# Performance work log

Hardware: AMD Instinct MI355X
Metric: run time of the kernel (lower is better)

Reference implementation:

```python
import jax, jax.numpy as jnp
import numpy as np

NEG_SLOPE = 0.2  # LeakyReLU slope used by GAT attention
EPS = 1e-16


def gat_conv(x, edge_index, W, a_src, a_dst, b):
    """One GATConv layer with 'mean' head aggregation.
    x: [N, Fin], edge_index: [2, E] (row 0 = src/j, row 1 = dst/i),
    W: [Fin, H*F], a_src/a_dst: [H, F], b: [F].
    Returns [N, F].
    """
    N = x.shape[0]
    H, F = a_src.shape
    h = (x @ W).reshape(N, H, F)                      # [N, H, F]
    src, dst = edge_index[0], edge_index[1]
    # per-node attention halves, gathered per edge
    as_ = jnp.einsum('nhf,hf->nh', h, a_src)          # [N, H]
    ad_ = jnp.einsum('nhf,hf->nh', h, a_dst)          # [N, H]
    e = jax.nn.leaky_relu(as_[src] + ad_[dst], NEG_SLOPE)  # [E, H]
    # segment softmax over incoming edges of each dst node
    m = jax.ops.segment_max(e, dst, num_segments=N)   # [N, H]
    ex = jnp.exp(e - m[dst])                          # [E, H]
    denom = jax.ops.segment_sum(ex, dst, num_segments=N)
    alpha = ex / (denom[dst] + EPS)                   # [E, H]
    # weighted scatter-aggregate of source features
    out = jax.ops.segment_sum(alpha[:, :, None] * h[src], dst, num_segments=N)  # [N, H, F]
    return out.mean(axis=1) + b                       # mean over heads


def setup_inputs() -> dict:
    key = jax.random.key(0)
    ks = jax.random.split(key, 10)
    N, E = 100000, 1000000
    in_dim, hid, out_dim, H = 128, 32, 16, 4
    x = jax.random.normal(ks[0], (N, in_dim), dtype=jnp.float32)
    edge_index = jax.random.randint(ks[1], (2, E), 0, N, dtype=jnp.int64)
    s1 = 1.0 / np.sqrt(in_dim)
    s2 = 1.0 / np.sqrt(hid)
    W1 = jax.random.uniform(ks[2], (in_dim, H * hid), jnp.float32, -s1, s1)
    a1_src = jax.random.uniform(ks[3], (H, hid), jnp.float32, -s2, s2)
    a1_dst = jax.random.uniform(ks[4], (H, hid), jnp.float32, -s2, s2)
    b1 = jnp.zeros((hid,), jnp.float32)
    s3 = 1.0 / np.sqrt(out_dim)
    W2 = jax.random.uniform(ks[5], (hid, H * out_dim), jnp.float32, -s2, s2)
    a2_src = jax.random.uniform(ks[6], (H, out_dim), jnp.float32, -s3, s3)
    a2_dst = jax.random.uniform(ks[7], (H, out_dim), jnp.float32, -s3, s3)
    b2 = jnp.zeros((out_dim,), jnp.float32)
    return {"x": x, "edge_index": edge_index,
            "W1": W1, "a1_src": a1_src, "a1_dst": a1_dst, "b1": b1,
            "W2": W2, "a2_src": a2_src, "a2_dst": a2_dst, "b2": b2}


def reference(x, edge_index, W1, a1_src, a1_dst, b1, W2, a2_src, a2_dst, b2):
    h = gat_conv(x, edge_index, W1, a1_src, a1_dst, b1)
    h = jax.nn.relu(h)
    # dropout is identity in eval mode
    out = gat_conv(h, edge_index, W2, a2_src, a2_dst, b2)
    return out
```

## Files before the change

kernel.cpp:

```cpp
#include <hip/hip_runtime.h>
#include <math.h>

#define NEG_SLOPE 0.2f
#define EPS_GAT 1e-16f
#define LOG2E 1.4426950408889634f
typedef unsigned int u32;
typedef unsigned short u16;
typedef __attribute__((ext_vector_type(8))) short short8;
typedef __attribute__((ext_vector_type(4))) float f32x4;

__device__ inline u16 f2bf(float x) {
    union { float f; u32 u; } v; v.f = x;
    u32 r = v.u + 0x7FFFu + ((v.u >> 16) & 1u);
    return (u16)(r >> 16);
}
__device__ inline float bf_lo(u32 u) {
    union { u32 i; float f; } v; v.i = u << 16; return v.f;
}
__device__ inline float bf_hi(u32 u) {
    union { u32 i; float f; } v; v.i = u & 0xFFFF0000u; return v.f;
}
__device__ inline float bf1(u16 s) {
    union { u32 i; float f; } v; v.i = ((u32)s) << 16; return v.f;
}
__device__ inline float fast_exp2(float x) {
#if __has_builtin(__builtin_amdgcn_exp2f)
    return __builtin_amdgcn_exp2f(x);
#else
    return exp2f(x);
#endif
}
__device__ inline float lrelu_exp2(float t) {
    return fast_exp2(fmaxf(t, NEG_SLOPE * t));
}


__global__ void degree_prep_kernel(const int* __restrict__ dst, int E,
                                   int* __restrict__ counts, int* __restrict__ rank,
                                   const float* __restrict__ W1,
                                   u16* __restrict__ w1t_hi, u16* __restrict__ w1t_lo,
                                   const float* __restrict__ W2, const float* __restrict__ a2s,
                                   const float* __restrict__ a2d, float* __restrict__ w_as,
                                   float* __restrict__ w_ad, int degBlocks) {
    int b = blockIdx.x;
    if (b < degBlocks) {
        int e = b * 256 + threadIdx.x;
        if (e < E) rank[e] = atomicAdd(&counts[dst[e]], 1);
    } else if (b < degBlocks + 64) {
        int i = (b - degBlocks) * 256 + threadIdx.x;
        int k = i >> 7, n = i & 127;
        float w = W1[i];
        u16 hi = f2bf(w);
        u16 lo = f2bf(w - bf1(hi));
        w1t_hi[n * 128 + k] = hi;
        w1t_lo[n * 128 + k] = lo;
    } else {
        int t = threadIdx.x;
        if (t < 128) {
            int h = t >> 5, k = t & 31;
            float s1 = 0.f, s2 = 0.f;
#pragma unroll
            for (int f = 0; f < 16; ++f) {
                float w = W2[k * 64 + h * 16 + f];
                s1 += w * a2s[h * 16 + f];
                s2 += w * a2d[h * 16 + f];
            }
            w_as[h * 32 + k] = s1;
            w_ad[h * 32 + k] = s2;
        }
    }
}

__global__ __launch_bounds__(1024) void scan_block_kernel(const int* __restrict__ counts, int N,
                                                          int* __restrict__ scanned, int* __restrict__ bsums) {
    __shared__ int tmp[1024];
    int i = blockIdx.x * 1024 + threadIdx.x;
    int v = (i < N) ? counts[i] : 0;
    tmp[threadIdx.x] = v;
    __syncthreads();
    for (int d = 1; d < 1024; d <<= 1) {
        int t = (threadIdx.x >= d) ? tmp[threadIdx.x - d] : 0;
        __syncthreads();
        tmp[threadIdx.x] += t;
        __syncthreads();
    }
    if (i < N) scanned[i] = tmp[threadIdx.x];
    if (threadIdx.x == 1023) bsums[blockIdx.x] = tmp[1023];
}

__global__ __launch_bounds__(256) void scan_partials_kernel(int* __restrict__ bsums, int nb) {
    __shared__ int tmp[256];
    int tid = threadIdx.x;
    int v = (tid < nb) ? bsums[tid] : 0;
    tmp[tid] = v;
    __syncthreads();
    for (int d = 1; d < 256; d <<= 1) {
        int t = (tid >= d) ? tmp[tid - d] : 0;
        __syncthreads();
        tmp[tid] += t;
        __syncthreads();
    }
    if (tid < nb) bsums[tid] = tmp[tid] - v;
}

__global__ void finalize_offsets_kernel(const int* __restrict__ scanned,
                                        const int* __restrict__ bsums_excl, int N,
                                        int* __restrict__ row_off) {
    int i = blockIdx.x * blockDim.x + threadIdx.x;
    if (i < N) {
        int incl = scanned[i] + bsums_excl[i >> 10];
        row_off[i + 1] = incl;
        if (i == 0) row_off[0] = 0;
    }
}

__global__ void fill_csr_kernel(const int* __restrict__ src, const int* __restrict__ dst, int E,
                                const int* __restrict__ row_off, const int* __restrict__ rank,
                                int* __restrict__ csr_src) {
    int e = blockIdx.x * blockDim.x + threadIdx.x;
    if (e < E) {
        int pos = row_off[dst[e]] + rank[e];
        csr_src[pos] = src[e];
    }
}


__global__ __launch_bounds__(256) void gemm1_mfma_kernel(const float* __restrict__ X,
                                                         const u16* __restrict__ w1t_hi,
                                                         const u16* __restrict__ w1t_lo,
                                                         const float* __restrict__ a_src,
                                                         const float* __restrict__ a_dst,
                                                         u16* __restrict__ Hb,
                                                         float* __restrict__ as_,
                                                         float* __restrict__ ad_, int N) {
    __shared__ u16 xsh_hi[64][40];
    __shared__ u16 xsh_lo[64][40];
    __shared__ u16 wbuf[10240];
    __shared__ float ash[128], adsh[128];
    u16* wsh_hi = wbuf;
    u16* wsh_lo = wbuf + 5120;
    int tid = threadIdx.x;
    int wave = tid >> 6, lane = tid & 63, quad = lane >> 4;
    int m0 = blockIdx.x * 64;

    if (tid < 128) { ash[tid] = a_src[tid]; adsh[tid] = a_dst[tid]; }

    f32x4 acc[4][2];
#pragma unroll
    for (int rt = 0; rt < 4; ++rt)
#pragma unroll
        for (int ct = 0; ct < 2; ++ct) acc[rt][ct] = (f32x4)(0.f);

    int xrow = tid >> 2, xkq = (tid & 3) * 8;

    for (int k0 = 0; k0 < 128; k0 += 32) {
        {
            int gr = m0 + xrow;
            float f[8];
            *(float4*)&f[0] = (gr < N) ? *(const float4*)(X + (size_t)gr * 128 + k0 + xkq)
                                       : make_float4(0.f, 0.f, 0.f, 0.f);
            *(float4*)&f[4] = (gr < N) ? *(const float4*)(X + (size_t)gr * 128 + k0 + xkq + 4)
                                       : make_float4(0.f, 0.f, 0.f, 0.f);
            u16 hi[8], lo[8];
#pragma unroll
            for (int i = 0; i < 8; ++i) {
                hi[i] = f2bf(f[i]);
                lo[i] = f2bf(f[i] - bf1(hi[i]));
            }
            *(uint4*)&xsh_hi[xrow][xkq] = *(uint4*)hi;
            *(uint4*)&xsh_lo[xrow][xkq] = *(uint4*)lo;
        }
        {
#pragma unroll
            for (int i = 0; i < 2; ++i) {
                int id = tid * 2 + i;
                int n = id >> 2, part = id & 3;
                *(uint4*)&wsh_hi[n * 40 + part * 8] =
                    ((const uint4*)(w1t_hi + n * 128 + k0))[part];
                *(uint4*)&wsh_lo[n * 40 + part * 8] =
                    ((const uint4*)(w1t_lo + n * 128 + k0))[part];
            }
        }
        __syncthreads();

        short8 bhi[2], blo[2];
#pragma unroll
        for (int ct = 0; ct < 2; ++ct) {
            int n = wave * 32 + ct * 16 + (lane & 15);
            bhi[ct] = *(const short8*)&wsh_hi[n * 40 + quad * 8];
            blo[ct] = *(const short8*)&wsh_lo[n * 40 + quad * 8];
        }
#pragma unroll
        for (int rt = 0; rt < 4; ++rt) {
            int m = rt * 16 + (lane & 15);
            short8 ahi = *(const short8*)&xsh_hi[m][quad * 8];
            short8 alo = *(const short8*)&xsh_lo[m][quad * 8];
#pragma unroll
            for (int ct = 0; ct < 2; ++ct) {
                acc[rt][ct] = __builtin_amdgcn_mfma_f32_16x16x32_bf16(ahi, bhi[ct], acc[rt][ct], 0, 0, 0);
                acc[rt][ct] = __builtin_amdgcn_mfma_f32_16x16x32_bf16(alo, bhi[ct], acc[rt][ct], 0, 0, 0);
                acc[rt][ct] = __builtin_amdgcn_mfma_f32_16x16x32_bf16(ahi, blo[ct], acc[rt][ct], 0, 0, 0);
            }
        }
        __syncthreads();
    }

    const int HS = 130;
#pragma unroll
    for (int rt = 0; rt < 4; ++rt)
#pragma unroll
        for (int ct = 0; ct < 2; ++ct) {
            int col = wave * 32 + ct * 16 + (lane & 15);
#pragma unroll
            for (int r = 0; r < 4; ++r) {
                int row = rt * 16 + quad * 4 + r;
                u16 hv = f2bf(acc[rt][ct][r]);
                int gr = m0 + row;
                if (gr < N) Hb[(size_t)gr * 128 + col] = hv;
                wbuf[row * HS + col] = hv;
            }
        }
    __syncthreads();

    {
        int row = tid >> 2, h = tid & 3;
        int gr = m0 + row;
        if (gr < N) {
            const u32* hr = (const u32*)&wbuf[row * HS + h * 32];
            float s1 = 0.f, s2 = 0.f;
#pragma unroll
            for (int q = 0; q < 16; ++q) {
                u32 u = hr[q];
                float flo = bf_lo(u), fhi = bf_hi(u);
                s1 += flo * ash[h * 32 + 2 * q] + fhi * ash[h * 32 + 2 * q + 1];
                s2 += flo * adsh[h * 32 + 2 * q] + fhi * adsh[h * 32 + 2 * q + 1];
            }
            as_[(size_t)gr * 4 + h] = s1 * LOG2E;
            ad_[(size_t)gr * 4 + h] = s2 * LOG2E;
        }
    }
}


__global__ __launch_bounds__(256) void node_agg128_kernel(const u32* __restrict__ Hb,
                                                          const float* __restrict__ as_,
                                                          const float* __restrict__ ad_,
                                                          const int* __restrict__ row_off,
                                                          const int* __restrict__ csr_src,
                                                          const float* __restrict__ bias,
                                                          const float* __restrict__ w_as,
                                                          const float* __restrict__ w_ad,
                                                          u32* __restrict__ O1,
                                                          float* __restrict__ as2,
                                                          float* __restrict__ ad2, int N) {
    int lane = threadIdx.x & 63;
    int node = __builtin_amdgcn_readfirstlane(blockIdx.x * 4 + (threadIdx.x >> 6));
    if (node >= N) return;
    int start = __builtin_amdgcn_readfirstlane(row_off[node]);
    int end   = __builtin_amdgcn_readfirstlane(row_off[node + 1]);
    int deg = end - start;
    int h = lane >> 4;
    int r = lane & 15;
    int grpbase = lane & 48;
    float adh = ad_[node * 4 + h];

    int clamp = (deg > 0) ? deg - 1 : 0;
    int vidx = (deg > 0) ? csr_src[start + min(lane, clamp)] : 0;
    int m = min(deg, 64);

    float Pv[4];
#pragma unroll
    for (int q = 0; q < 4; ++q) {
        int eq = q * 16 + r;
        int sq = __shfl(vidx, eq);
        float aq = as_[sq * 4 + h];
        float pe = lrelu_exp2(aq + adh);
        Pv[q] = (eq < m) ? pe : 0.f;
    }
    float den = (Pv[0] + Pv[1]) + (Pv[2] + Pv[3]);
    den += __shfl_xor(den, 1);
    den += __shfl_xor(den, 2);
    den += __shfl_xor(den, 4);
    den += __shfl_xor(den, 8);

    float2 acc = make_float2(0.f, 0.f);
    int j = 0;
#pragma unroll
    for (int q = 0; q < 4; ++q) {
        const int lim = min(m, (q + 1) * 16);
        for (; j + 4 <= lim; j += 4) {
            int s0 = __builtin_amdgcn_readlane(vidx, j);
            int s1 = __builtin_amdgcn_readlane(vidx, j + 1);
            int s2 = __builtin_amdgcn_readlane(vidx, j + 2);
            int s3 = __builtin_amdgcn_readlane(vidx, j + 3);
            float e0 = __shfl(Pv[q], grpbase | (j - q * 16));
            float e1 = __shfl(Pv[q], grpbase | (j + 1 - q * 16));
            float e2 = __shfl(Pv[q], grpbase | (j + 2 - q * 16));
            float e3 = __shfl(Pv[q], grpbase | (j + 3 - q * 16));
            u32 u0 = Hb[(size_t)s0 * 64 + lane];
            u32 u1 = Hb[(size_t)s1 * 64 + lane];
            u32 u2 = Hb[(size_t)s2 * 64 + lane];
            u32 u3 = Hb[(size_t)s3 * 64 + lane];
            acc.x = fmaf(e0, bf_lo(u0), acc.x); acc.y = fmaf(e0, bf_hi(u0), acc.y);
            acc.x = fmaf(e1, bf_lo(u1), acc.x); acc.y = fmaf(e1, bf_hi(u1), acc.y);
            acc.x = fmaf(e2, bf_lo(u2), acc.x); acc.y = fmaf(e2, bf_hi(u2), acc.y);
            acc.x = fmaf(e3, bf_lo(u3), acc.x); acc.y = fmaf(e3, bf_hi(u3), acc.y);
        }
        for (; j < lim; ++j) {
            int s = __builtin_amdgcn_readlane(vidx, j);
            float e = __shfl(Pv[q], grpbase | (j - q * 16));
            u32 u = Hb[(size_t)s * 64 + lane];
            acc.x = fmaf(e, bf_lo(u), acc.x); acc.y = fmaf(e, bf_hi(u), acc.y);
        }
    }
    for (int jj = start + 64; jj < end; ++jj) {
        int s = __builtin_amdgcn_readfirstlane(csr_src[jj]);
        float e = lrelu_exp2(as_[s * 4 + h] + adh);
        u32 u = Hb[(size_t)s * 64 + lane];
        acc.x = fmaf(e, bf_lo(u), acc.x); acc.y = fmaf(e, bf_hi(u), acc.y); den += e;
    }
    float inv = 1.f / (den + EPS_GAT);
    float px = acc.x * inv, py = acc.y * inv;
    px += __shfl_xor(px, 16); py += __shfl_xor(py, 16);
    px += __shfl_xor(px, 32); py += __shfl_xor(py, 32);

    int f2 = (lane & 15) * 2;
    float2 bv = *(const float2*)&bias[f2];
    float ox = fmaxf(px * 0.25f + bv.x, 0.f);
    float oy = fmaxf(py * 0.25f + bv.y, 0.f);
    if (lane < 16)
        O1[node * 16 + lane] = (u32)f2bf(ox) | ((u32)f2bf(oy) << 16);

    int h2 = lane >> 4;
    float2 wa = *(const float2*)&w_as[h2 * 32 + f2];
    float2 wd = *(const float2*)&w_ad[h2 * 32 + f2];
    float ta = ox * wa.x + oy * wa.y;
    float td = ox * wd.x + oy * wd.y;
    ta += __shfl_xor(ta, 1); td += __shfl_xor(td, 1);
    ta += __shfl_xor(ta, 2); td += __shfl_xor(td, 2);
    ta += __shfl_xor(ta, 4); td += __shfl_xor(td, 4);
    ta += __shfl_xor(ta, 8); td += __shfl_xor(td, 8);
    if ((lane & 15) == 0) {
        as2[node * 4 + h2] = ta * LOG2E;
        ad2[node * 4 + h2] = td * LOG2E;
    }
}


__global__ __launch_bounds__(256) void node_agg32_fused_kernel(const u32* __restrict__ O1,
                                                               const float* __restrict__ as_,
                                                               const float* __restrict__ ad_,
                                                               const int* __restrict__ row_off,
                                                               const int* __restrict__ csr_src,
                                                               const float* __restrict__ W2,
                                                               const float* __restrict__ b2,
                                                               float* __restrict__ Out, int N) {
    int lane = threadIdx.x & 63;
    int h = lane >> 4, f = lane & 15;
    int grpbase = lane & 48;
    int node = __builtin_amdgcn_readfirstlane(blockIdx.x * 4 + (threadIdx.x >> 6));
    if (node >= N) return;

    float wcol[32];
#pragma unroll
    for (int k = 0; k < 32; ++k) wcol[k] = W2[k * 64 + lane];
    float bo = b2[f];

    int start = __builtin_amdgcn_readfirstlane(row_off[node]);
    int end   = __builtin_amdgcn_readfirstlane(row_off[node + 1]);
    int deg = end - start;
    float adh = ad_[node * 4 + h];

    int clamp = (deg > 0) ? deg - 1 : 0;
    int vidx = (deg > 0) ? csr_src[start + min(lane, clamp)] : 0;
    int m = min(deg, 64);

    float Pv[4];
#pragma unroll
    for (int q = 0; q < 4; ++q) {
        int eq = q * 16 + f;
        int sq = __shfl(vidx, eq);
        float aq = as_[sq * 4 + h];
        float pe = lrelu_exp2(aq + adh);
        Pv[q] = (eq < m) ? pe : 0.f;
    }
    float den = (Pv[0] + Pv[1]) + (Pv[2] + Pv[3]);
    den += __shfl_xor(den, 1);
    den += __shfl_xor(den, 2);
    den += __shfl_xor(den, 4);
    den += __shfl_xor(den, 8);

    float2 acc = make_float2(0.f, 0.f);
    int j = 0;
#pragma unroll
    for (int q = 0; q < 4; ++q) {
        const int lim = min(m, (q + 1) * 16);
        for (; j + 4 <= lim; j += 4) {
            int s0 = __builtin_amdgcn_readlane(vidx, j);
            int s1 = __builtin_amdgcn_readlane(vidx, j + 1);
            int s2 = __builtin_amdgcn_readlane(vidx, j + 2);
            int s3 = __builtin_amdgcn_readlane(vidx, j + 3);
            float e0 = __shfl(Pv[q], grpbase | (j - q * 16));
            float e1 = __shfl(Pv[q], grpbase | (j + 1 - q * 16));
            float e2 = __shfl(Pv[q], grpbase | (j + 2 - q * 16));
            float e3 = __shfl(Pv[q], grpbase | (j + 3 - q * 16));
            u32 u0 = O1[s0 * 16 + f];
            u32 u1 = O1[s1 * 16 + f];
            u32 u2 = O1[s2 * 16 + f];
            u32 u3 = O1[s3 * 16 + f];
            acc.x = fmaf(e0, bf_lo(u0), acc.x); acc.y = fmaf(e0, bf_hi(u0), acc.y);
            acc.x = fmaf(e1, bf_lo(u1), acc.x); acc.y = fmaf(e1, bf_hi(u1), acc.y);
            acc.x = fmaf(e2, bf_lo(u2), acc.x); acc.y = fmaf(e2, bf_hi(u2), acc.y);
            acc.x = fmaf(e3, bf_lo(u3), acc.x); acc.y = fmaf(e3, bf_hi(u3), acc.y);
        }
        for (; j < lim; ++j) {
            int s = __builtin_amdgcn_readlane(vidx, j);
            float e = __shfl(Pv[q], grpbase | (j - q * 16));
            u32 u = O1[s * 16 + f];
            acc.x = fmaf(e, bf_lo(u), acc.x); acc.y = fmaf(e, bf_hi(u), acc.y);
        }
    }
    for (int jj = start + 64; jj < end; ++jj) {
        int s = __builtin_amdgcn_readfirstlane(csr_src[jj]);
        float e = lrelu_exp2(as_[s * 4 + h] + adh);
        u32 u = O1[s * 16 + f];
        acc.x = fmaf(e, bf_lo(u), acc.x); acc.y = fmaf(e, bf_hi(u), acc.y);
        den += e;
    }
    float inv = 1.f / (den + EPS_GAT);
    float px = acc.x * inv, py = acc.y * inv;

    float s = 0.f;
#pragma unroll
    for (int k = 0; k < 16; ++k) {
        float vx = __shfl(px, grpbase | k);
        float vy = __shfl(py, grpbase | k);
        s = fmaf(vx, wcol[2 * k], s);
        s = fmaf(vy, wcol[2 * k + 1], s);
    }
    s += __shfl_xor(s, 16);
    s += __shfl_xor(s, 32);
    if (lane < 16)
        Out[(size_t)node * 16 + f] = s * 0.25f + bo;
}


extern "C" void kernel_launch(void* const* d_in, const int* in_sizes, int n_in,
                              void* d_out, int out_size, void* d_ws, size_t ws_size,
                              hipStream_t stream) {
    const float* x      = (const float*)d_in[0];
    const int*   eidx   = (const int*)d_in[1];
    const float* W1     = (const float*)d_in[2];
    const float* a1_src = (const float*)d_in[3];
    const float* a1_dst = (const float*)d_in[4];
    const float* b1     = (const float*)d_in[5];
    const float* W2     = (const float*)d_in[6];
    const float* a2_src = (const float*)d_in[7];
    const float* a2_dst = (const float*)d_in[8];
    const float* b2     = (const float*)d_in[9];
    float* out = (float*)d_out;

    const int N = in_sizes[0] / 128;
    const int E = in_sizes[1] / 2;
    const int* src = eidx;
    const int* dst = eidx + E;

    char* base = (char*)d_ws;
    size_t off = 0;
    auto carve = [&](size_t bytes) -> char* {
        off = (off + 255) & ~(size_t)255;
        char* p = base + off;
        off += bytes;
        return p;
    };
    int* counts   = (int*)carve((size_t)N * 4);
    int* scanned  = (int*)carve((size_t)N * 4);
    int* bsums    = (int*)carve(256 * 4);
    int* row_off  = (int*)carve((size_t)(N + 1) * 4);
    int* rank     = (int*)carve((size_t)E * 4);
    int* csr_src  = (int*)carve((size_t)E * 4);
    u16* w1t_hi   = (u16*)carve(128 * 128 * 2);
    u16* w1t_lo   = (u16*)carve(128 * 128 * 2);
    u16* h1b      = (u16*)carve((size_t)N * 128 * 2);
    u32* out1b    = (u32*)carve((size_t)N * 16 * 4);
    float* as1  = (float*)carve((size_t)N * 4 * 4);
    float* ad1  = (float*)carve((size_t)N * 4 * 4);
    float* as2  = (float*)carve((size_t)N * 4 * 4);
    float* ad2  = (float*)carve((size_t)N * 4 * 4);
    float* w_as = (float*)carve(4 * 32 * 4);
    float* w_ad = (float*)carve(4 * 32 * 4);
    (void)ws_size; (void)n_in; (void)out_size;

    hipMemsetAsync(counts, 0, (size_t)N * 4, stream);
    int degBlocks = (E + 255) / 256;
    degree_prep_kernel<<<degBlocks + 65, 256, 0, stream>>>(dst, E, counts, rank,
                                                           W1, w1t_hi, w1t_lo,
                                                           W2, a2_src, a2_dst, w_as, w_ad,
                                                           degBlocks);
    int nb = (N + 1023) / 1024;
    scan_block_kernel<<<nb, 1024, 0, stream>>>(counts, N, scanned, bsums);
    scan_partials_kernel<<<1, 256, 0, stream>>>(bsums, nb);
    finalize_offsets_kernel<<<(N + 255) / 256, 256, 0, stream>>>(scanned, bsums, N, row_off);
    fill_csr_kernel<<<(E + 255) / 256, 256, 0, stream>>>(src, dst, E, row_off, rank, csr_src);

    gemm1_mfma_kernel<<<(N + 63) / 64, 256, 0, stream>>>(x, w1t_hi, w1t_lo, a1_src, a1_dst,
                                                         h1b, as1, ad1, N);
    node_agg128_kernel<<<(N + 3) / 4, 256, 0, stream>>>((const u32*)h1b, as1, ad1,
                                                        row_off, csr_src, b1, w_as, w_ad,
                                                        out1b, as2, ad2, N);

    node_agg32_fused_kernel<<<(N + 3) / 4, 256, 0, stream>>>(out1b, as2, ad2, row_off,
                                                             csr_src, W2, b2, out, N);
}
```

Measured before the change: 315.5 us.

## Specialize low-degree aggregation paths and stage W2 in shared memory

Both aggregation kernels get fast paths for nodes with up to 8 or up to 16 in-edges. These paths compute only the first quarter of attention scores and issue eight gathers back-to-back before accumulating, which puts more loads in flight and skips the unused score slots. Nodes with higher degree keep the original general loop. In the second-layer kernel, the 32-register per-lane copy of W2 is replaced by a block-wide copy of W2 in LDS, read during the output projection. This is meant to cut register pressure and raise occupancy, at the cost of a barrier and extra LDS traffic per block.

```diff
diff --git a/kernel.cpp b/kernel.cpp
--- a/kernel.cpp
+++ b/kernel.cpp
@@ -268,57 +268,96 @@
     int vidx = (deg > 0) ? csr_src[start + min(lane, clamp)] : 0;
     int m = min(deg, 64);
 
-    float Pv[4];
-#pragma unroll
-    for (int q = 0; q < 4; ++q) {
-        int eq = q * 16 + r;
-        int sq = __shfl(vidx, eq);
+    float Pv0;
+    {
+        int sq = __shfl(vidx, r);
         float aq = as_[sq * 4 + h];
         float pe = lrelu_exp2(aq + adh);
-        Pv[q] = (eq < m) ? pe : 0.f;
-    }
-    float den = (Pv[0] + Pv[1]) + (Pv[2] + Pv[3]);
+        Pv0 = (r < m) ? pe : 0.f;
+    }
+    float den = Pv0;
     den += __shfl_xor(den, 1);
     den += __shfl_xor(den, 2);
     den += __shfl_xor(den, 4);
     den += __shfl_xor(den, 8);
 
     float2 acc = make_float2(0.f, 0.f);
-    int j = 0;
-#pragma unroll
-    for (int q = 0; q < 4; ++q) {
-        const int lim = min(m, (q + 1) * 16);
-        for (; j + 4 <= lim; j += 4) {
-            int s0 = __builtin_amdgcn_readlane(vidx, j);
-            int s1 = __builtin_amdgcn_readlane(vidx, j + 1);
-            int s2 = __builtin_amdgcn_readlane(vidx, j + 2);
-            int s3 = __builtin_amdgcn_readlane(vidx, j + 3);
-            float e0 = __shfl(Pv[q], grpbase | (j - q * 16));
-            float e1 = __shfl(Pv[q], grpbase | (j + 1 - q * 16));
-            float e2 = __shfl(Pv[q], grpbase | (j + 2 - q * 16));
-            float e3 = __shfl(Pv[q], grpbase | (j + 3 - q * 16));
-            u32 u0 = Hb[(size_t)s0 * 64 + lane];
-            u32 u1 = Hb[(size_t)s1 * 64 + lane];
-            u32 u2 = Hb[(size_t)s2 * 64 + lane];
-            u32 u3 = Hb[(size_t)s3 * 64 + lane];
-            acc.x = fmaf(e0, bf_lo(u0), acc.x); acc.y = fmaf(e0, bf_hi(u0), acc.y);
-            acc.x = fmaf(e1, bf_lo(u1), acc.x); acc.y = fmaf(e1, bf_hi(u1), acc.y);
-            acc.x = fmaf(e2, bf_lo(u2), acc.x); acc.y = fmaf(e2, bf_hi(u2), acc.y);
-            acc.x = fmaf(e3, bf_lo(u3), acc.x); acc.y = fmaf(e3, bf_hi(u3), acc.y);
-        }
-        for (; j < lim; ++j) {
-            int s = __builtin_amdgcn_readlane(vidx, j);
-            float e = __shfl(Pv[q], grpbase | (j - q * 16));
+
+#define AGG128_BLK8(J0)                                                           \
+    {                                                                             \
+        int sj[8]; u32 uj[8];                                                     \
+        _Pragma("unroll") for (int j = 0; j < 8; ++j)                             \
+            sj[j] = __builtin_amdgcn_readlane(vidx, (J0) + j);                    \
+        _Pragma("unroll") for (int j = 0; j < 8; ++j)                             \
+            uj[j] = Hb[(size_t)sj[j] * 64 + lane];                                \
+        _Pragma("unroll") for (int j = 0; j < 8; ++j) {                           \
+            float e = __shfl(Pv0, grpbase | ((J0) + j));                          \
+            acc.x = fmaf(e, bf_lo(uj[j]), acc.x);                                 \
+            acc.y = fmaf(e, bf_hi(uj[j]), acc.y);                                 \
+        }                                                                         \
+    }
+
+    if (m <= 8) {
+        AGG128_BLK8(0)
+    } else if (m <= 16) {
+        AGG128_BLK8(0)
+        AGG128_BLK8(8)
+    } else {
+        float Pv[4];
+        Pv[0] = Pv0;
+#pragma unroll
+        for (int q = 1; q < 4; ++q) {
+            int eq = q * 16 + r;
+            int sq = __shfl(vidx, eq);
+            float aq = as_[sq * 4 + h];
+            float pe = lrelu_exp2(aq + adh);
+            Pv[q] = (eq < m) ? pe : 0.f;
+        }
+        float d2 = Pv[1] + Pv[2] + Pv[3];
+        d2 += __shfl_xor(d2, 1);
+        d2 += __shfl_xor(d2, 2);
+        d2 += __shfl_xor(d2, 4);
+        d2 += __shfl_xor(d2, 8);
+        den += d2;
+
+        int j = 0;
+#pragma unroll
+        for (int q = 0; q < 4; ++q) {
+            const int lim = min(m, (q + 1) * 16);
+            for (; j + 4 <= lim; j += 4) {
+                int s0 = __builtin_amdgcn_readlane(vidx, j);
+                int s1 = __builtin_amdgcn_readlane(vidx, j + 1);
+                int s2 = __builtin_amdgcn_readlane(vidx, j + 2);
+                int s3 = __builtin_amdgcn_readlane(vidx, j + 3);
+                float e0 = __shfl(Pv[q], grpbase | (j - q * 16));
+                float e1 = __shfl(Pv[q], grpbase | (j + 1 - q * 16));
+                float e2 = __shfl(Pv[q], grpbase | (j + 2 - q * 16));
+                float e3 = __shfl(Pv[q], grpbase | (j + 3 - q * 16));
+                u32 u0 = Hb[(size_t)s0 * 64 + lane];
+                u32 u1 = Hb[(size_t)s1 * 64 + lane];
+                u32 u2 = Hb[(size_t)s2 * 64 + lane];
+                u32 u3 = Hb[(size_t)s3 * 64 + lane];
+                acc.x = fmaf(e0, bf_lo(u0), acc.x); acc.y = fmaf(e0, bf_hi(u0), acc.y);
+                acc.x = fmaf(e1, bf_lo(u1), acc.x); acc.y = fmaf(e1, bf_hi(u1), acc.y);
+                acc.x = fmaf(e2, bf_lo(u2), acc.x); acc.y = fmaf(e2, bf_hi(u2), acc.y);
+                acc.x = fmaf(e3, bf_lo(u3), acc.x); acc.y = fmaf(e3, bf_hi(u3), acc.y);
+            }
+            for (; j < lim; ++j) {
+                int s = __builtin_amdgcn_readlane(vidx, j);
+                float e = __shfl(Pv[q], grpbase | (j - q * 16));
+                u32 u = Hb[(size_t)s * 64 + lane];
+                acc.x = fmaf(e, bf_lo(u), acc.x); acc.y = fmaf(e, bf_hi(u), acc.y);
+            }
+        }
+        for (int jj = start + 64; jj < end; ++jj) {
+            int s = __builtin_amdgcn_readfirstlane(csr_src[jj]);
+            float e = lrelu_exp2(as_[s * 4 + h] + adh);
             u32 u = Hb[(size_t)s * 64 + lane];
-            acc.x = fmaf(e, bf_lo(u), acc.x); acc.y = fmaf(e, bf_hi(u), acc.y);
-        }
-    }
-    for (int jj = start + 64; jj < end; ++jj) {
-        int s = __builtin_amdgcn_readfirstlane(csr_src[jj]);
-        float e = lrelu_exp2(as_[s * 4 + h] + adh);
-        u32 u = Hb[(size_t)s * 64 + lane];
-        acc.x = fmaf(e, bf_lo(u), acc.x); acc.y = fmaf(e, bf_hi(u), acc.y); den += e;
-    }
+            acc.x = fmaf(e, bf_lo(u), acc.x); acc.y = fmaf(e, bf_hi(u), acc.y); den += e;
+        }
+    }
+#undef AGG128_BLK8
+
     float inv = 1.f / (den + EPS_GAT);
     float px = acc.x * inv, py = acc.y * inv;
     px += __shfl_xor(px, 16); py += __shfl_xor(py, 16);
@@ -355,16 +394,21 @@
                                                                const float* __restrict__ W2,
                                                                const float* __restrict__ b2,
                                                                float* __restrict__ Out, int N) {
-    int lane = threadIdx.x & 63;
+    __shared__ float w2sh[2048];
+    int tid = threadIdx.x;
+    {
+        float4 v = ((const float4*)W2)[tid];
+        *(float4*)&w2sh[tid * 4] = v;
+        float4 v2 = ((const float4*)W2)[tid + 256];
+        *(float4*)&w2sh[(tid + 256) * 4] = v2;
+    }
+    __syncthreads();
+
+    int lane = tid & 63;
     int h = lane >> 4, f = lane & 15;
     int grpbase = lane & 48;
-    int node = __builtin_amdgcn_readfirstlane(blockIdx.x * 4 + (threadIdx.x >> 6));
+    int node = __builtin_amdgcn_readfirstlane(blockIdx.x * 4 + (tid >> 6));
     if (node >= N) return;
-
-    float wcol[32];
-#pragma unroll
-    for (int k = 0; k < 32; ++k) wcol[k] = W2[k * 64 + lane];
-    float bo = b2[f];
 
     int start = __builtin_amdgcn_readfirstlane(row_off[node]);
     int end   = __builtin_amdgcn_readfirstlane(row_off[node + 1]);
@@ -375,58 +419,97 @@
     int vidx = (deg > 0) ? csr_src[start + min(lane, clamp)] : 0;
     int m = min(deg, 64);
 
-    float Pv[4];
-#pragma unroll
-    for (int q = 0; q < 4; ++q) {
-        int eq = q * 16 + f;
-        int sq = __shfl(vidx, eq);
+    float Pv0;
+    {
+        int sq = __shfl(vidx, f);
         float aq = as_[sq * 4 + h];
         float pe = lrelu_exp2(aq + adh);
-        Pv[q] = (eq < m) ? pe : 0.f;
-    }
-    float den = (Pv[0] + Pv[1]) + (Pv[2] + Pv[3]);
+        Pv0 = (f < m) ? pe : 0.f;
+    }
+    float den = Pv0;
     den += __shfl_xor(den, 1);
     den += __shfl_xor(den, 2);
     den += __shfl_xor(den, 4);
     den += __shfl_xor(den, 8);
 
     float2 acc = make_float2(0.f, 0.f);
-    int j = 0;
-#pragma unroll
-    for (int q = 0; q < 4; ++q) {
-        const int lim = min(m, (q + 1) * 16);
-        for (; j + 4 <= lim; j += 4) {
-            int s0 = __builtin_amdgcn_readlane(vidx, j);
-            int s1 = __builtin_amdgcn_readlane(vidx, j + 1);
-            int s2 = __builtin_amdgcn_readlane(vidx, j + 2);
-            int s3 = __builtin_amdgcn_readlane(vidx, j + 3);
-            float e0 = __shfl(Pv[q], grpbase | (j - q * 16));
-            float e1 = __shfl(Pv[q], grpbase | (j + 1 - q * 16));
-            float e2 = __shfl(Pv[q], grpbase | (j + 2 - q * 16));
-            float e3 = __shfl(Pv[q], grpbase | (j + 3 - q * 16));
-            u32 u0 = O1[s0 * 16 + f];
-            u32 u1 = O1[s1 * 16 + f];
-            u32 u2 = O1[s2 * 16 + f];
-            u32 u3 = O1[s3 * 16 + f];
-            acc.x = fmaf(e0, bf_lo(u0), acc.x); acc.y = fmaf(e0, bf_hi(u0), acc.y);
-            acc.x = fmaf(e1, bf_lo(u1), acc.x); acc.y = fmaf(e1, bf_hi(u1), acc.y);
-            acc.x = fmaf(e2, bf_lo(u2), acc.x); acc.y = fmaf(e2, bf_hi(u2), acc.y);
-            acc.x = fmaf(e3, bf_lo(u3), acc.x); acc.y = fmaf(e3, bf_hi(u3), acc.y);
-        }
-        for (; j < lim; ++j) {
-            int s = __builtin_amdgcn_readlane(vidx, j);
-            float e = __shfl(Pv[q], grpbase | (j - q * 16));
+
+#define AGG32_BLK8(J0)                                                            \
+    {                                                                             \
+        int sj[8]; u32 uj[8];                                                     \
+        _Pragma("unroll") for (int j = 0; j < 8; ++j)                             \
+            sj[j] = __builtin_amdgcn_readlane(vidx, (J0) + j);                    \
+        _Pragma("unroll") for (int j = 0; j < 8; ++j)                             \
+            uj[j] = O1[(size_t)sj[j] * 16 + f];                                   \
+        _Pragma("unroll") for (int j = 0; j < 8; ++j) {                           \
+            float e = __shfl(Pv0, grpbase | ((J0) + j));                          \
+            acc.x = fmaf(e, bf_lo(uj[j]), acc.x);                                 \
+            acc.y = fmaf(e, bf_hi(uj[j]), acc.y);                                 \
+        }                                                                         \
+    }
+
+    if (m <= 8) {
+        AGG32_BLK8(0)
+    } else if (m <= 16) {
+        AGG32_BLK8(0)
+        AGG32_BLK8(8)
+    } else {
+        float Pv[4];
+        Pv[0] = Pv0;
+#pragma unroll
+        for (int q = 1; q < 4; ++q) {
+            int eq = q * 16 + f;
+            int sq = __shfl(vidx, eq);
+            float aq = as_[sq * 4 + h];
+            float pe = lrelu_exp2(aq + adh);
+            Pv[q] = (eq < m) ? pe : 0.f;
+        }
+        float d2 = Pv[1] + Pv[2] + Pv[3];
+        d2 += __shfl_xor(d2, 1);
+        d2 += __shfl_xor(d2, 2);
+        d2 += __shfl_xor(d2, 4);
+        d2 += __shfl_xor(d2, 8);
+        den += d2;
+
+        int j = 0;
+#pragma unroll
+        for (int q = 0; q < 4; ++q) {
+            const int lim = min(m, (q + 1) * 16);
+            for (; j + 4 <= lim; j += 4) {
+                int s0 = __builtin_amdgcn_readlane(vidx, j);
+                int s1 = __builtin_amdgcn_readlane(vidx, j + 1);
+                int s2 = __builtin_amdgcn_readlane(vidx, j + 2);
+                int s3 = __builtin_amdgcn_readlane(vidx, j + 3);
+                float e0 = __shfl(Pv[q], grpbase | (j - q * 16));
+                float e1 = __shfl(Pv[q], grpbase | (j + 1 - q * 16));
+                float e2 = __shfl(Pv[q], grpbase | (j + 2 - q * 16));
+                float e3 = __shfl(Pv[q], grpbase | (j + 3 - q * 16));
+                u32 u0 = O1[s0 * 16 + f];
+                u32 u1 = O1[s1 * 16 + f];
+                u32 u2 = O1[s2 * 16 + f];
+                u32 u3 = O1[s3 * 16 + f];
+                acc.x = fmaf(e0, bf_lo(u0), acc.x); acc.y = fmaf(e0, bf_hi(u0), acc.y);
+                acc.x = fmaf(e1, bf_lo(u1), acc.x); acc.y = fmaf(e1, bf_hi(u1), acc.y);
+                acc.x = fmaf(e2, bf_lo(u2), acc.x); acc.y = fmaf(e2, bf_hi(u2), acc.y);
+                acc.x = fmaf(e3, bf_lo(u3), acc.x); acc.y = fmaf(e3, bf_hi(u3), acc.y);
+            }
+            for (; j < lim; ++j) {
+                int s = __builtin_amdgcn_readlane(vidx, j);
+                float e = __shfl(Pv[q], grpbase | (j - q * 16));
+                u32 u = O1[s * 16 + f];
+                acc.x = fmaf(e, bf_lo(u), acc.x); acc.y = fmaf(e, bf_hi(u), acc.y);
+            }
+        }
+        for (int jj = start + 64; jj < end; ++jj) {
+            int s = __builtin_amdgcn_readfirstlane(csr_src[jj]);
+            float e = lrelu_exp2(as_[s * 4 + h] + adh);
             u32 u = O1[s * 16 + f];
             acc.x = fmaf(e, bf_lo(u), acc.x); acc.y = fmaf(e, bf_hi(u), acc.y);
-        }
-    }
-    for (int jj = start + 64; jj < end; ++jj) {
-        int s = __builtin_amdgcn_readfirstlane(csr_src[jj]);
-        float e = lrelu_exp2(as_[s * 4 + h] + adh);
-        u32 u = O1[s * 16 + f];
-        acc.x = fmaf(e, bf_lo(u), acc.x); acc.y = fmaf(e, bf_hi(u), acc.y);
-        den += e;
-    }
+            den += e;
+        }
+    }
+#undef AGG32_BLK8
+
     float inv = 1.f / (den + EPS_GAT);
     float px = acc.x * inv, py = acc.y * inv;
 
@@ -435,13 +518,13 @@
     for (int k = 0; k < 16; ++k) {
         float vx = __shfl(px, grpbase | k);
         float vy = __shfl(py, grpbase | k);
-        s = fmaf(vx, wcol[2 * k], s);
-        s = fmaf(vy, wcol[2 * k + 1], s);
+        s = fmaf(vx, w2sh[(2 * k) * 64 + lane], s);
+        s = fmaf(vy, w2sh[(2 * k + 1) * 64 + lane], s);
     }
     s += __shfl_xor(s, 16);
     s += __shfl_xor(s, 32);
     if (lane < 16)
-        Out[(size_t)node * 16 + f] = s * 0.25f + bo;
+        Out[(size_t)node * 16 + f] = s * 0.25f + b2[f];
 }
 
 
```

Measured after the change: 311.4 us. No clear change (-1.3%).
